# Kernel tuning notes

Hardware: AMD Instinct MI355X
Metric: run time of the kernel (lower is better)

The kernel has to match this reference:

```python
import jax, jax.numpy as jnp
import numpy as np

N_VOX = 200000   # active input voxels
M_VOX = 100000   # active output voxels
K_VOL = 27       # 3x3x3 kernel offsets
C_IN = 32
C_OUT = 64


def setup_inputs() -> dict:
    key = jax.random.key(0)
    k1, k2, k3, k4 = jax.random.split(key, 4)
    feats = jax.random.normal(k1, (N_VOX, C_IN), dtype=jnp.float32)
    # kernel init ~ U(-std, std), std = 1/sqrt(in_channels * kernel_volume)
    std = 1.0 / np.sqrt(C_IN * K_VOL)
    kernel = jax.random.uniform(k2, (K_VOL, C_IN, C_OUT), dtype=jnp.float32,
                                minval=-std, maxval=std)
    # kernel map: for each offset k and output voxel m, an input voxel index
    in_idx = jax.random.randint(k3, (K_VOL, M_VOX), 0, N_VOX, dtype=jnp.int32)
    # occupancy mask: 1 if that (offset, output) pair exists in the kernel map
    mask = jax.random.randint(k4, (K_VOL, M_VOX), 0, 2, dtype=jnp.int32)
    return {"feats": feats, "kernel": kernel, "in_idx": in_idx, "mask": mask}


def reference(feats, kernel, in_idx, mask) -> jnp.ndarray:
    # Gather neighbor features per kernel offset: [K, M, C_in]
    gathered = feats[in_idx]
    gathered = gathered * mask[..., None].astype(feats.dtype)
    # Per-offset GEMM + scatter-add (offsets align on output voxels, so the
    # scatter-add is a sum over the K axis): [M, C_out]
    out = jnp.einsum('kmi,kio->mo', gathered, kernel)
    return out
```

## Files before the change

kernel.cpp:

```cpp
#include <hip/hip_runtime.h>

#define M_VOX   100000
#define N_VOX   200000
#define K_VOL   27
#define C_IN    32
#define C_OUT   64
#define DEPTH   14

typedef __bf16 bf16x8 __attribute__((ext_vector_type(8)));
typedef float  floatx4 __attribute__((ext_vector_type(4)));

#define FEATSB_BYTES  ((N_VOX + 1) * C_IN * 2)
#define BFRAG_OFF     FEATSB_BYTES

#define FEAT_CHUNKS   ((N_VOX + 1) * 4)
#define FEAT_BLOCKS   ((FEAT_CHUNKS + 255) / 256)
__global__ __launch_bounds__(256) void prep_all(
    const float* __restrict__ feats, const float* __restrict__ kernelw,
    __bf16* __restrict__ featsB, bf16x8* __restrict__ Bfrag)
{
    if (blockIdx.x < FEAT_BLOCKS) {
        const int c = blockIdx.x * 256 + threadIdx.x;
        if (c >= FEAT_CHUNKS) return;
        bf16x8 v;
        if (c < N_VOX * 4) {
            floatx4 f0 = *(const floatx4*)(feats + c * 8);
            floatx4 f1 = *(const floatx4*)(feats + c * 8 + 4);
#pragma unroll
            for (int j = 0; j < 4; ++j) { v[j] = (__bf16)f0[j]; v[4 + j] = (__bf16)f1[j]; }
        } else {
#pragma unroll
            for (int j = 0; j < 8; ++j) v[j] = (__bf16)0.0f;
        }
        *(bf16x8*)(featsB + c * 8) = v;
    } else {
        const int k    = blockIdx.x - FEAT_BLOCKS;
        const int tid  = threadIdx.x;
        const int tile = tid >> 6;
        const int col  = tid & 15;
        const int quad = (tid >> 4) & 3;
        const float* kp = kernelw + k * C_IN * C_OUT + quad * 8 * C_OUT + tile * 16 + col;
        bf16x8 b;
#pragma unroll
        for (int j = 0; j < 8; ++j) b[j] = (__bf16)kp[j * C_OUT];
        Bfrag[k * 256 + tid] = b;
    }
}

__global__ __launch_bounds__(256, 3) void sparse_conv_mfma(
    const __bf16* __restrict__ featsB,
    const bf16x8* __restrict__ Bfrag,
    const int* __restrict__ in_idx,
    const int* __restrict__ mask,
    float* __restrict__ out)
{
    const int tid  = threadIdx.x;
    const int lane = tid & 63;
    const int wv   = tid >> 6;
    const int col  = lane & 15;
    const int quad = lane >> 4;

    const int m0 = blockIdx.x * 64 + wv * 16;
    if (m0 >= M_VOX) return;

    int mi[K_VOL];
#pragma unroll
    for (int k = 0; k < K_VOL; ++k) {
        const int ix = in_idx[k * M_VOX + m0 + col];
        const int mk = mask[k * M_VOX + m0 + col];
        mi[k] = mk ? ix : N_VOX;
    }

    const __bf16* fbase = featsB + quad * 8;

    bf16x8 A[DEPTH];
#pragma unroll
    for (int k = 0; k < DEPTH; ++k)
        A[k] = *(const bf16x8*)(fbase + (size_t)mi[k] * C_IN);

    floatx4 acc0 = {0.f,0.f,0.f,0.f}, acc1 = {0.f,0.f,0.f,0.f};
    floatx4 acc2 = {0.f,0.f,0.f,0.f}, acc3 = {0.f,0.f,0.f,0.f};

    const bf16x8* bbase = Bfrag + lane;
    bf16x8 nb0 = bbase[0*64], nb1 = bbase[1*64], nb2 = bbase[2*64], nb3 = bbase[3*64];

#pragma unroll
    for (int k = 0; k < K_VOL; ++k) {
        const int s = k % DEPTH;
        bf16x8 a  = A[s];
        bf16x8 b0 = nb0, b1 = nb1, b2 = nb2, b3 = nb3;

        if (k + DEPTH < K_VOL)
            A[s] = *(const bf16x8*)(fbase + (size_t)mi[k + DEPTH] * C_IN);
        if (k + 1 < K_VOL) {
            const bf16x8* bb = bbase + (k + 1) * 256;
            nb0 = bb[0*64]; nb1 = bb[1*64]; nb2 = bb[2*64]; nb3 = bb[3*64];
        }

        acc0 = __builtin_amdgcn_mfma_f32_16x16x32_bf16(a, b0, acc0, 0, 0, 0);
        acc1 = __builtin_amdgcn_mfma_f32_16x16x32_bf16(a, b1, acc1, 0, 0, 0);
        acc2 = __builtin_amdgcn_mfma_f32_16x16x32_bf16(a, b2, acc2, 0, 0, 0);
        acc3 = __builtin_amdgcn_mfma_f32_16x16x32_bf16(a, b3, acc3, 0, 0, 0);
    }

    float* op = out + (size_t)(m0 + quad * 4) * C_OUT + col;
#pragma unroll
    for (int r = 0; r < 4; ++r) {
        op[r * C_OUT + 0]  = acc0[r];
        op[r * C_OUT + 16] = acc1[r];
        op[r * C_OUT + 32] = acc2[r];
        op[r * C_OUT + 48] = acc3[r];
    }
}

extern "C" void kernel_launch(void* const* d_in, const int* in_sizes, int n_in,
                              void* d_out, int out_size, void* d_ws, size_t ws_size,
                              hipStream_t stream) {
    const float* feats   = (const float*)d_in[0];
    const float* kernelw = (const float*)d_in[1];
    const int*   in_idx  = (const int*)d_in[2];
    const int*   maskp   = (const int*)d_in[3];
    float*       out     = (float*)d_out;

    __bf16* featsB = (__bf16*)d_ws;
    bf16x8* BfragP = (bf16x8*)((char*)d_ws + BFRAG_OFF);

    prep_all<<<dim3(FEAT_BLOCKS + K_VOL), dim3(256), 0, stream>>>(
        feats, kernelw, featsB, BfragP);

    const int blocks = (M_VOX + 63) / 64;
    sparse_conv_mfma<<<dim3(blocks), dim3(256), 0, stream>>>(
        featsB, BfragP, in_idx, maskp, out);
}
```

Measured before the change: 137.2 us.

## Stage weight fragments in LDS across 1024-thread blocks with two-phase loading

Weight fragments now go into shared memory in two halves (14 offsets, then 13), with block-wide barriers between phases, so 16 waves share them instead of each wave loading from global. Blocks grow to 1024 threads covering 256 voxels. The deep 14-entry register prefetch of gathered features is replaced by a single-step prefetch, which cuts register pressure but exposes more gather latency. The barriers in the middle of the K loop also serialize the waves.

```diff
diff --git a/kernel.cpp b/kernel.cpp
--- a/kernel.cpp
+++ b/kernel.cpp
@@ -5,7 +5,10 @@
 #define K_VOL   27
 #define C_IN    32
 #define C_OUT   64
-#define DEPTH   14
+
+#define STG0        14
+#define BLK_THREADS 1024
+#define VOX_PER_BLK 256
 
 typedef __bf16 bf16x8 __attribute__((ext_vector_type(8)));
 typedef float  floatx4 __attribute__((ext_vector_type(4)));
@@ -47,69 +50,94 @@
     }
 }
 
-__global__ __launch_bounds__(256, 3) void sparse_conv_mfma(
+__global__ __launch_bounds__(BLK_THREADS) void sparse_conv_mfma(
     const __bf16* __restrict__ featsB,
-    const bf16x8* __restrict__ Bfrag,
+    const bf16x8* __restrict__ BfragG,
     const int* __restrict__ in_idx,
     const int* __restrict__ mask,
     float* __restrict__ out)
 {
+    __shared__ bf16x8 ldsB[STG0 * 256];
+
     const int tid  = threadIdx.x;
     const int lane = tid & 63;
     const int wv   = tid >> 6;
     const int col  = lane & 15;
     const int quad = lane >> 4;
 
-    const int m0 = blockIdx.x * 64 + wv * 16;
-    if (m0 >= M_VOX) return;
+    const int m0 = blockIdx.x * VOX_PER_BLK + wv * 16;
+    const bool active = (m0 < M_VOX);
+
+#pragma unroll 2
+    for (int i = tid; i < STG0 * 256; i += BLK_THREADS) ldsB[i] = BfragG[i];
 
     int mi[K_VOL];
+    if (active) {
 #pragma unroll
-    for (int k = 0; k < K_VOL; ++k) {
-        const int ix = in_idx[k * M_VOX + m0 + col];
-        const int mk = mask[k * M_VOX + m0 + col];
-        mi[k] = mk ? ix : N_VOX;
+        for (int k = 0; k < K_VOL; ++k) {
+            const int ix = in_idx[k * M_VOX + m0 + col];
+            const int mk = mask[k * M_VOX + m0 + col];
+            mi[k] = mk ? ix : N_VOX;
+        }
     }
-
-    const __bf16* fbase = featsB + quad * 8;
-
-    bf16x8 A[DEPTH];
-#pragma unroll
-    for (int k = 0; k < DEPTH; ++k)
-        A[k] = *(const bf16x8*)(fbase + (size_t)mi[k] * C_IN);
+    __syncthreads();
 
     floatx4 acc0 = {0.f,0.f,0.f,0.f}, acc1 = {0.f,0.f,0.f,0.f};
     floatx4 acc2 = {0.f,0.f,0.f,0.f}, acc3 = {0.f,0.f,0.f,0.f};
 
-    const bf16x8* bbase = Bfrag + lane;
-    bf16x8 nb0 = bbase[0*64], nb1 = bbase[1*64], nb2 = bbase[2*64], nb3 = bbase[3*64];
+    const __bf16*  fbase = featsB + quad * 8;
+    const bf16x8*  lbase = ldsB + lane;
 
+    bf16x8 a_n;
+    if (active) a_n = *(const bf16x8*)(fbase + (size_t)mi[0] * C_IN);
+
+    if (active) {
 #pragma unroll
-    for (int k = 0; k < K_VOL; ++k) {
-        const int s = k % DEPTH;
-        bf16x8 a  = A[s];
-        bf16x8 b0 = nb0, b1 = nb1, b2 = nb2, b3 = nb3;
+        for (int k = 0; k < STG0; ++k) {
+            bf16x8 a  = a_n;
+            bf16x8 b0 = lbase[k * 256 + 0 * 64];
+            bf16x8 b1 = lbase[k * 256 + 1 * 64];
+            bf16x8 b2 = lbase[k * 256 + 2 * 64];
+            bf16x8 b3 = lbase[k * 256 + 3 * 64];
+            if (k + 1 < K_VOL)
+                a_n = *(const bf16x8*)(fbase + (size_t)mi[k + 1] * C_IN);
+            acc0 = __builtin_amdgcn_mfma_f32_16x16x32_bf16(a, b0, acc0, 0, 0, 0);
+            acc1 = __builtin_amdgcn_mfma_f32_16x16x32_bf16(a, b1, acc1, 0, 0, 0);
+            acc2 = __builtin_amdgcn_mfma_f32_16x16x32_bf16(a, b2, acc2, 0, 0, 0);
+            acc3 = __builtin_amdgcn_mfma_f32_16x16x32_bf16(a, b3, acc3, 0, 0, 0);
+        }
+    }
 
-        if (k + DEPTH < K_VOL)
-            A[s] = *(const bf16x8*)(fbase + (size_t)mi[k + DEPTH] * C_IN);
-        if (k + 1 < K_VOL) {
-            const bf16x8* bb = bbase + (k + 1) * 256;
-            nb0 = bb[0*64]; nb1 = bb[1*64]; nb2 = bb[2*64]; nb3 = bb[3*64];
+    __syncthreads();
+#pragma unroll 2
+    for (int i = tid; i < (K_VOL - STG0) * 256; i += BLK_THREADS)
+        ldsB[i] = BfragG[STG0 * 256 + i];
+    __syncthreads();
+
+    if (active) {
+#pragma unroll
+        for (int k = STG0; k < K_VOL; ++k) {
+            bf16x8 a  = a_n;
+            bf16x8 b0 = lbase[(k - STG0) * 256 + 0 * 64];
+            bf16x8 b1 = lbase[(k - STG0) * 256 + 1 * 64];
+            bf16x8 b2 = lbase[(k - STG0) * 256 + 2 * 64];
+            bf16x8 b3 = lbase[(k - STG0) * 256 + 3 * 64];
+            if (k + 1 < K_VOL)
+                a_n = *(const bf16x8*)(fbase + (size_t)mi[k + 1] * C_IN);
+            acc0 = __builtin_amdgcn_mfma_f32_16x16x32_bf16(a, b0, acc0, 0, 0, 0);
+            acc1 = __builtin_amdgcn_mfma_f32_16x16x32_bf16(a, b1, acc1, 0, 0, 0);
+            acc2 = __builtin_amdgcn_mfma_f32_16x16x32_bf16(a, b2, acc2, 0, 0, 0);
+            acc3 = __builtin_amdgcn_mfma_f32_16x16x32_bf16(a, b3, acc3, 0, 0, 0);
         }
 
-        acc0 = __builtin_amdgcn_mfma_f32_16x16x32_bf16(a, b0, acc0, 0, 0, 0);
-        acc1 = __builtin_amdgcn_mfma_f32_16x16x32_bf16(a, b1, acc1, 0, 0, 0);
-        acc2 = __builtin_amdgcn_mfma_f32_16x16x32_bf16(a, b2, acc2, 0, 0, 0);
-        acc3 = __builtin_amdgcn_mfma_f32_16x16x32_bf16(a, b3, acc3, 0, 0, 0);
-    }
-
-    float* op = out + (size_t)(m0 + quad * 4) * C_OUT + col;
+        float* op = out + (size_t)(m0 + quad * 4) * C_OUT + col;
 #pragma unroll
-    for (int r = 0; r < 4; ++r) {
-        op[r * C_OUT + 0]  = acc0[r];
-        op[r * C_OUT + 16] = acc1[r];
-        op[r * C_OUT + 32] = acc2[r];
-        op[r * C_OUT + 48] = acc3[r];
+        for (int r = 0; r < 4; ++r) {
+            op[r * C_OUT + 0]  = acc0[r];
+            op[r * C_OUT + 16] = acc1[r];
+            op[r * C_OUT + 32] = acc2[r];
+            op[r * C_OUT + 48] = acc3[r];
+        }
     }
 }
 
@@ -128,7 +156,7 @@
     prep_all<<<dim3(FEAT_BLOCKS + K_VOL), dim3(256), 0, stream>>>(
         feats, kernelw, featsB, BfragP);
 
-    const int blocks = (M_VOX + 63) / 64;
-    sparse_conv_mfma<<<dim3(blocks), dim3(256), 0, stream>>>(
+    const int blocks = (M_VOX + VOX_PER_BLK - 1) / VOX_PER_BLK;
+    sparse_conv_mfma<<<dim3(blocks), dim3(BLK_THREADS), 0, stream>>>(
         featsB, BfragP, in_idx, maskp, out);
 }
```

After: 122.1 us. -11.0%, faster.
